# Optimization experiments

Measured on AMD Instinct MI355X. Metric: run time of the kernel, lower is better.

## Reference

```python
import jax, jax.numpy as jnp
import numpy as np

B, T, H = 2, 4096, 2048
NH, DK, DV = 16, 128, 128
CONV = 4
MLP_H = 32
EPS_STAT = 1e-6   # surprise_stat_eps
NORM_EPS = 1e-5   # o_norm eps
L2_EPS = 1e-6     # qk l2norm eps in kernel


def setup_inputs() -> dict:
    key = jax.random.key(0)
    ks = jax.random.split(key, 20)
    def w(k, shape, scale=None):
        scale = (1.0 / np.sqrt(shape[-1])) if scale is None else scale
        return jax.random.normal(k, shape, jnp.float32) * scale
    return dict(
        hidden_states=jax.random.normal(ks[0], (B, T, H), jnp.float32),
        Wq=w(ks[1], (NH * DK, H)),
        Wk=w(ks[2], (NH * DK, H)),
        Wv=w(ks[3], (NH * DV, H)),
        conv_q=w(ks[4], (NH * DK, CONV), 0.5),
        conv_k=w(ks[5], (NH * DK, CONV), 0.5),
        conv_v=w(ks[6], (NH * DV, CONV), 0.5),
        A_log=jnp.log(jax.random.uniform(ks[7], (NH,), jnp.float32, 1.0, 16.0)),
        dt_bias=jnp.zeros((NH * DK,), jnp.float32),
        Wsv=w(ks[8], (DV, DK)),
        Wb1=w(ks[9], (MLP_H, 3)), bb1=jnp.zeros((MLP_H,), jnp.float32),
        Wb2=w(ks[10], (1, MLP_H)), bb2=jnp.zeros((1,), jnp.float32),
        Wa1=w(ks[11], (MLP_H, 3)), ba1=jnp.zeros((MLP_H,), jnp.float32),
        Wa2=w(ks[12], (1, MLP_H)), ba2=jnp.zeros((1,), jnp.float32),
        Wg1=w(ks[13], (DV, H)),
        Wg2=w(ks[14], (NH * DV, DV)), bg2=jnp.zeros((NH * DV,), jnp.float32),
        norm_w=jnp.ones((DV,), jnp.float32),
        Wo=w(ks[15], (H, NH * DV)),
    )


def short_conv(x, w):
    """Causal depthwise conv1d (kernel CONV, no bias) + silu. x: [B,T,C], w: [C,CONV]."""
    K = w.shape[-1]
    xp = jnp.pad(x, ((0, 0), (K - 1, 0), (0, 0)))
    y = sum(xp[:, i:i + x.shape[1], :] * w[:, i] for i in range(K))
    return jax.nn.silu(y)


def _mlp(s, W1, b1, W2, b2):
    return (jax.nn.silu(s @ W1.T + b1) @ W2.T + b2)[..., 0]


def reference(hidden_states, Wq, Wk, Wv, conv_q, conv_k, conv_v, A_log, dt_bias,
              Wsv, Wb1, bb1, Wb2, bb2, Wa1, ba1, Wa2, ba2,
              Wg1, Wg2, bg2, norm_w, Wo):
    x = hidden_states
    Bsz, Tlen, _ = x.shape
    # projections + short conv + silu
    q = short_conv(x @ Wq.T, conv_q).reshape(Bsz, Tlen, NH, DK)
    k = short_conv(x @ Wk.T, conv_k).reshape(Bsz, Tlen, NH, DK)
    v = short_conv(x @ Wv.T, conv_v).reshape(Bsz, Tlen, NH, DV)

    # surprise proxy error stats
    v_hat = jnp.einsum('bthk,vk->bthv', k, Wsv)
    e = v_hat - v
    s_l2 = jnp.sqrt(jnp.sum(e * e, -1) + EPS_STAT)
    s_l1 = jnp.sum(jnp.abs(e), -1)
    cos_den = jnp.sqrt(jnp.sum(v_hat * v_hat, -1) + EPS_STAT) * \
              jnp.sqrt(jnp.sum(v * v, -1) + EPS_STAT) + EPS_STAT
    s_cos = 1.0 - jnp.sum(v_hat * v, -1) / cos_den
    s = jnp.stack([s_l2, s_l1, s_cos], -1)                 # [B,T,NH,3]

    beta = jax.nn.sigmoid(_mlp(s, Wb1, bb1, Wb2, bb2))      # [B,T,NH]
    amp = _mlp(s, Wa1, ba1, Wa2, ba2)                       # logit_normalizer = 1
    r = k / jnp.maximum(jnp.linalg.norm(k, axis=-1, keepdims=True), 1e-12)
    g_raw = r * amp[..., None]                              # [B,T,NH,DK]

    # KDA gate: g = -exp(A_log) * softplus(g_raw + dt_bias)
    g = -jnp.exp(A_log)[None, None, :, None] * \
        jax.nn.softplus(g_raw + dt_bias.reshape(NH, DK))

    # q/k l2-normalization inside kernel
    qn = q * jax.lax.rsqrt(jnp.sum(q * q, -1, keepdims=True) + L2_EPS)
    kn = k * jax.lax.rsqrt(jnp.sum(k * k, -1, keepdims=True) + L2_EPS)
    scale = DK ** -0.5

    def step(S, inp):
        q_t, k_t, v_t, g_t, b_t = inp                       # [B,NH,*]
        S = S * jnp.exp(g_t)[..., None]                     # per-key-dim decay, S:[B,NH,DK,DV]
        kv = jnp.einsum('bhk,bhkv->bhv', k_t, S)            # k^T S
        delta = (v_t - kv) * b_t[..., None]                 # surprise-gated delta update
        S = S + k_t[..., None] * delta[..., None, :]
        o_t = jnp.einsum('bhk,bhkv->bhv', q_t * scale, S)
        return S, o_t

    tfirst = lambda a: jnp.swapaxes(a, 0, 1)
    S0 = jnp.zeros((Bsz, NH, DK, DV), jnp.float32)
    _, o = jax.lax.scan(step, S0, (tfirst(qn), tfirst(kn), tfirst(v), tfirst(g), tfirst(beta)))
    o = jnp.swapaxes(o, 0, 1)                               # [B,T,NH,DV]

    # gated RMSNorm (sigmoid gate) + output proj
    gate = ((x @ Wg1.T) @ Wg2.T + bg2).reshape(Bsz, Tlen, NH, DV)
    o = o * jax.lax.rsqrt(jnp.mean(o * o, -1, keepdims=True) + NORM_EPS) * norm_w
    o = o * jax.nn.sigmoid(gate)
    return o.reshape(Bsz, Tlen, NH * DV) @ Wo.T
```

## Files before the change

### kernel.cpp

```cpp
#include <hip/hip_runtime.h>
#include <hip/hip_bf16.h>


typedef __attribute__((ext_vector_type(8))) short bf16x8;
typedef __attribute__((ext_vector_type(4))) short bf16x4;
typedef __attribute__((ext_vector_type(4))) float floatx4;

#define TB 4096
#define RSH 664
#define NREC 4096
#define BHSH ((size_t)NREC * RSH)
#define CSB ((size_t)16 * RSH * 2)

__device__ __forceinline__ float b2f(ushort u) {
    union { unsigned int u; float f; } c; c.u = ((unsigned int)u) << 16; return c.f;
}
__device__ __forceinline__ ushort f2b(float f) {
    union { float f; unsigned int u; } c; c.f = f;
    unsigned int r = (c.u + 0x7fffu + ((c.u >> 16) & 1u)) >> 16;
    return (ushort)r;
}
__device__ __forceinline__ float silu(float x) { return x / (1.0f + expf(-x)); }
__device__ __forceinline__ void dec8(uint4 u, float* f) {
    f[0] = __uint_as_float(u.x << 16); f[1] = __uint_as_float(u.x & 0xffff0000u);
    f[2] = __uint_as_float(u.y << 16); f[3] = __uint_as_float(u.y & 0xffff0000u);
    f[4] = __uint_as_float(u.z << 16); f[5] = __uint_as_float(u.z & 0xffff0000u);
    f[6] = __uint_as_float(u.w << 16); f[7] = __uint_as_float(u.w & 0xffff0000u);
}
__device__ __forceinline__ void dec4(uint2 u, float* f) {
    f[0] = __uint_as_float(u.x << 16); f[1] = __uint_as_float(u.x & 0xffff0000u);
    f[2] = __uint_as_float(u.y << 16); f[3] = __uint_as_float(u.y & 0xffff0000u);
}
__device__ __forceinline__ bf16x4 asbf(uint2 u) {
    union { uint2 a; bf16x4 b; } c; c.a = u; return c.b;
}

#if __has_builtin(__builtin_amdgcn_mfma_f32_16x16x16bf16_1k)
__device__ __forceinline__ floatx4 MFMA16(bf16x4 a, bf16x4 b, floatx4 c) {
    return __builtin_amdgcn_mfma_f32_16x16x16bf16_1k(a, b, c, 0, 0, 0);
}
#else
__device__ __forceinline__ floatx4 MFMA16(bf16x4 a, bf16x4 b, floatx4 c) {
    asm volatile("v_mfma_f32_16x16x16_bf16 %0, %1, %2, %0\n\ts_nop 7\n\ts_nop 7"
                 : "+v"(c) : "v"(a), "v"(b));
    return c;
}
#endif

__global__ __launch_bounds__(256) void cast_f32_bf16(const float* __restrict__ in,
                                                     ushort* __restrict__ out, int n) {
    int i = (blockIdx.x * 256 + threadIdx.x) * 4;
    int stride = gridDim.x * 256 * 4;
    for (; i + 3 < n; i += stride) {
        float4 v = *(const float4*)(in + i);
        ushort4 u;
        u.x = f2b(v.x); u.y = f2b(v.y); u.z = f2b(v.z); u.w = f2b(v.w);
        *(ushort4*)(out + i) = u;
    }
}

template <typename CT>
__global__ __launch_bounds__(256) void gemm_bf16(const ushort* __restrict__ A,
                                                 const ushort* __restrict__ B,
                                                 CT* __restrict__ C, int M, int N, int K) {
    __shared__ ushort As[128 * 40];
    __shared__ ushort Bs[128 * 40];
    const int tid = threadIdx.x;
    const int lane = tid & 63, wid = tid >> 6;
    const int wr = wid >> 1, wc = wid & 1;
    const int bm = blockIdx.y, bn = blockIdx.x;

    const int r0 = tid >> 2;
    const int kc0 = (tid & 3) * 8;
    const size_t aoff0 = (size_t)(bm * 128 + r0) * K + kc0;
    const size_t aoff1 = aoff0 + (size_t)64 * K;
    const size_t boff0 = (size_t)(bn * 128 + r0) * K + kc0;
    const size_t boff1 = boff0 + (size_t)64 * K;
    const int lw0 = r0 * 40 + kc0;
    const int lw1 = (r0 + 64) * 40 + kc0;

    const int arow = wr * 64 + (lane & 15);
    const int brow = wc * 64 + (lane & 15);
    const int kg = (lane >> 4) * 8;

    floatx4 acc[4][4];
#pragma unroll
    for (int m = 0; m < 4; ++m)
#pragma unroll
        for (int n = 0; n < 4; ++n) acc[m][n] = (floatx4){0.f, 0.f, 0.f, 0.f};

    uint4 ra0 = *(const uint4*)(A + aoff0);
    uint4 ra1 = *(const uint4*)(A + aoff1);
    uint4 rb0 = *(const uint4*)(B + boff0);
    uint4 rb1 = *(const uint4*)(B + boff1);

    for (int kt = 32; kt <= K; kt += 32) {
        __syncthreads();
        *(uint4*)(As + lw0) = ra0;
        *(uint4*)(As + lw1) = ra1;
        *(uint4*)(Bs + lw0) = rb0;
        *(uint4*)(Bs + lw1) = rb1;
        __syncthreads();
        if (kt < K) {
            ra0 = *(const uint4*)(A + aoff0 + kt);
            ra1 = *(const uint4*)(A + aoff1 + kt);
            rb0 = *(const uint4*)(B + boff0 + kt);
            rb1 = *(const uint4*)(B + boff1 + kt);
        }
        bf16x8 af[4], bfr[4];
#pragma unroll
        for (int m = 0; m < 4; ++m) af[m] = *(const bf16x8*)(As + (arow + m * 16) * 40 + kg);
#pragma unroll
        for (int n = 0; n < 4; ++n) bfr[n] = *(const bf16x8*)(Bs + (brow + n * 16) * 40 + kg);
#pragma unroll
        for (int m = 0; m < 4; ++m)
#pragma unroll
            for (int n = 0; n < 4; ++n)
                acc[m][n] = __builtin_amdgcn_mfma_f32_16x16x32_bf16(af[m], bfr[n], acc[m][n], 0, 0, 0);
    }

    const int crow0 = bm * 128 + wr * 64 + (lane >> 4) * 4;
    const int ccol0 = bn * 128 + wc * 64 + (lane & 15);
#pragma unroll
    for (int m = 0; m < 4; ++m)
#pragma unroll
        for (int n = 0; n < 4; ++n)
#pragma unroll
            for (int j = 0; j < 4; ++j) {
                int row = crow0 + m * 16 + j;
                int col = ccol0 + n * 16;
                if constexpr (sizeof(CT) == 2)
                    C[(size_t)row * N + col] = (CT)f2b(acc[m][n][j]);
                else
                    C[(size_t)row * N + col] = (CT)acc[m][n][j];
            }
}

__global__ __launch_bounds__(256) void conv_stats_kernel(
    const ushort* __restrict__ qkv,
    const float* __restrict__ convq, const float* __restrict__ convk,
    const float* __restrict__ convv, const float* __restrict__ Wsv,
    const float* __restrict__ Wb1, const float* __restrict__ bb1,
    const float* __restrict__ Wb2, const float* __restrict__ bb2,
    const float* __restrict__ Wa1, const float* __restrict__ ba1,
    const float* __restrict__ Wa2, const float* __restrict__ ba2,
    const float* __restrict__ A_log, const float* __restrict__ dt_bias,
    ushort* __restrict__ P) {
    __shared__ ushort wsv_s[128 * 136];
    __shared__ float k_sh[4][128];
    for (int i = threadIdx.x; i < 128 * 128; i += 256) {
        int row = i >> 7, col = i & 127;
        wsv_s[row * 136 + col] = f2b(Wsv[i]);
    }
    __syncthreads();
    const int wid = threadIdx.x >> 6, lane = threadIdx.x & 63;

    for (int it = 0; it < 2; ++it) {
        const int pair = blockIdx.x * 8 + it * 4 + wid;
        const int t = pair >> 4, h = pair & 15;
        const int c0 = h * 128 + 2 * lane, c1 = c0 + 1;

        float wq[4], wq2[4], wk[4], wk2[4], wv[4], wv2[4];
#pragma unroll
        for (int i2 = 0; i2 < 4; ++i2) {
            wq[i2] = convq[c0 * 4 + i2]; wq2[i2] = convq[c1 * 4 + i2];
            wk[i2] = convk[c0 * 4 + i2]; wk2[i2] = convk[c1 * 4 + i2];
            wv[i2] = convv[c0 * 4 + i2]; wv2[i2] = convv[c1 * 4 + i2];
        }
        float aq0 = 0, aq1 = 0, ak0 = 0, ak1 = 0, av0 = 0, av1 = 0;
#pragma unroll
        for (int i2 = 0; i2 < 4; ++i2) {
            int tt = t - 3 + i2;
            if (tt >= 0) {
                const ushort* rowp = qkv + (size_t)tt * 6144 + h * 128;
                uint xq = *(const uint*)(rowp + 2 * lane);
                uint xk = *(const uint*)(rowp + 2048 + 2 * lane);
                uint xv = *(const uint*)(rowp + 4096 + 2 * lane);
                aq0 = fmaf(__uint_as_float(xq << 16), wq[i2], aq0);
                aq1 = fmaf(__uint_as_float(xq & 0xffff0000u), wq2[i2], aq1);
                ak0 = fmaf(__uint_as_float(xk << 16), wk[i2], ak0);
                ak1 = fmaf(__uint_as_float(xk & 0xffff0000u), wk2[i2], ak1);
                av0 = fmaf(__uint_as_float(xv << 16), wv[i2], av0);
                av1 = fmaf(__uint_as_float(xv & 0xffff0000u), wv2[i2], av1);
            }
        }
        float q0 = silu(aq0), q1 = silu(aq1);
        float k0 = silu(ak0), k1 = silu(ak1);
        float v0 = silu(av0), v1 = silu(av1);

        __syncthreads();
        k_sh[wid][2 * lane] = k0;
        k_sh[wid][2 * lane + 1] = k1;
        __syncthreads();

        float vh0 = 0.f, vh1 = 0.f;
        const ushort* wr0 = wsv_s + (2 * lane) * 136;
        const ushort* wr1 = wsv_s + (2 * lane + 1) * 136;
#pragma unroll 4
        for (int j = 0; j < 128; j += 8) {
            float4 ka = *(const float4*)&k_sh[wid][j];
            float4 kb = *(const float4*)&k_sh[wid][j + 4];
            uint4 wa = *(const uint4*)(wr0 + j);
            uint4 wb = *(const uint4*)(wr1 + j);
            vh0 = fmaf(__uint_as_float(wa.x << 16), ka.x, vh0);
            vh0 = fmaf(__uint_as_float(wa.x & 0xffff0000u), ka.y, vh0);
            vh0 = fmaf(__uint_as_float(wa.y << 16), ka.z, vh0);
            vh0 = fmaf(__uint_as_float(wa.y & 0xffff0000u), ka.w, vh0);
            vh0 = fmaf(__uint_as_float(wa.z << 16), kb.x, vh0);
            vh0 = fmaf(__uint_as_float(wa.z & 0xffff0000u), kb.y, vh0);
            vh0 = fmaf(__uint_as_float(wa.w << 16), kb.z, vh0);
            vh0 = fmaf(__uint_as_float(wa.w & 0xffff0000u), kb.w, vh0);
            vh1 = fmaf(__uint_as_float(wb.x << 16), ka.x, vh1);
            vh1 = fmaf(__uint_as_float(wb.x & 0xffff0000u), ka.y, vh1);
            vh1 = fmaf(__uint_as_float(wb.y << 16), ka.z, vh1);
            vh1 = fmaf(__uint_as_float(wb.y & 0xffff0000u), ka.w, vh1);
            vh1 = fmaf(__uint_as_float(wb.z << 16), kb.x, vh1);
            vh1 = fmaf(__uint_as_float(wb.z & 0xffff0000u), kb.y, vh1);
            vh1 = fmaf(__uint_as_float(wb.w << 16), kb.z, vh1);
            vh1 = fmaf(__uint_as_float(wb.w & 0xffff0000u), kb.w, vh1);
        }

        float e0 = vh0 - v0, e1 = vh1 - v1;
        float se2 = e0 * e0 + e1 * e1;
        float sl1 = fabsf(e0) + fabsf(e1);
        float shv = vh0 * v0 + vh1 * v1;
        float shh = vh0 * vh0 + vh1 * vh1;
        float svv = v0 * v0 + v1 * v1;
        float sk2 = k0 * k0 + k1 * k1;
        float sq2 = q0 * q0 + q1 * q1;
#pragma unroll
        for (int m = 32; m >= 1; m >>= 1) {
            se2 += __shfl_xor(se2, m);
            sl1 += __shfl_xor(sl1, m);
            shv += __shfl_xor(shv, m);
            shh += __shfl_xor(shh, m);
            svv += __shfl_xor(svv, m);
            sk2 += __shfl_xor(sk2, m);
            sq2 += __shfl_xor(sq2, m);
        }
        float s_l2 = sqrtf(se2 + 1e-6f);
        float s_l1 = sl1;
        float s_cos = 1.0f - shv / (sqrtf(shh + 1e-6f) * sqrtf(svv + 1e-6f) + 1e-6f);

        const int j2 = lane & 31;
        const float* W1 = (lane < 32) ? Wb1 : Wa1;
        const float* b1 = (lane < 32) ? bb1 : ba1;
        const float* W2 = (lane < 32) ? Wb2 : Wa2;
        float pre = W1[j2 * 3] * s_l2 + W1[j2 * 3 + 1] * s_l1 + W1[j2 * 3 + 2] * s_cos + b1[j2];
        float val = W2[j2] * silu(pre);
#pragma unroll
        for (int m = 16; m >= 1; m >>= 1) val += __shfl_xor(val, m);
        float pre_b = __shfl(val, 0) + bb2[0];
        float pre_a = __shfl(val, 32) + ba2[0];
        float betav = 1.0f / (1.0f + expf(-pre_b));
        float amp = pre_a;

        float knorm = sqrtf(sk2);
        float rinv = amp / fmaxf(knorm, 1e-12f);
        float ah = expf(A_log[h]);
        float gr0 = fmaf(k0, rinv, dt_bias[c0]);
        float gr1 = fmaf(k1, rinv, dt_bias[c1]);
        float sp0 = (gr0 > 20.f) ? gr0 : log1pf(expf(gr0));
        float sp1 = (gr1 > 20.f) ? gr1 : log1pf(expf(gr1));

        ushort* rec = P + (size_t)h * BHSH + (size_t)t * RSH;
        float kinv = rsqrtf(sk2 + 1e-6f);
        float qinv = rsqrtf(sq2 + 1e-6f) * 0.08838834764831845f;
        *(uint*)(rec + 128 + 2 * lane) = (uint)f2b(q0 * qinv) | ((uint)f2b(q1 * qinv) << 16);
        *(uint*)(rec + 256 + 2 * lane) = (uint)f2b(k0 * kinv) | ((uint)f2b(k1 * kinv) << 16);
        *(uint*)(rec + 384 + 2 * lane) = (uint)f2b(expf(-ah * sp0)) | ((uint)f2b(expf(-ah * sp1)) << 16);
        *(uint*)(rec + 512 + 2 * lane) = (uint)f2b(v0) | ((uint)f2b(v1) << 16);
        if (lane == 0) *(float*)(rec + 640) = betav;
    }
}

__global__ __launch_bounds__(256, 1) void phasea_kernel(ushort* __restrict__ P) {
    __shared__ float lA[4][16][16];
    __shared__ float lU[4][16][16];
    __shared__ float lM[4][16][16];
    const int wid = threadIdx.x >> 6, lane = threadIdx.x & 63;
    const int g = blockIdx.x * 4 + wid;
    const int s = g >> 8, n = g & 255;
    ushort* cb = P + (size_t)s * BHSH + (size_t)n * (16 * RSH);
    char* sb = (char*)cb;
    float (*A_)[16] = lA[wid];
    float (*U_)[16] = lU[wid];
    float (*M_)[16] = lM[wid];

    float kf[32], Ef[32], qf[32], bf[16];
    uint vq[16];
#pragma unroll
    for (int i = 0; i < 16; ++i) {
        const ushort* r = cb + i * RSH;
        uint ku = *(const uint*)(r + 256 + 2 * lane);
        uint eu = *(const uint*)(r + 384 + 2 * lane);
        uint qu = *(const uint*)(r + 128 + 2 * lane);
        vq[i] = *(const uint*)(r + 512 + 2 * lane);
        bf[i] = *(const float*)(r + 640);
        kf[2 * i]     = __uint_as_float(ku << 16);
        kf[2 * i + 1] = __uint_as_float(ku & 0xffff0000u);
        Ef[2 * i]     = __uint_as_float(eu << 16);
        Ef[2 * i + 1] = __uint_as_float(eu & 0xffff0000u);
        qf[2 * i]     = __uint_as_float(qu << 16);
        qf[2 * i + 1] = __uint_as_float(qu & 0xffff0000u);
    }

    float R[32];
    float Pc0 = 1.f, Pc1 = 1.f;
#pragma unroll
    for (int i = 0; i < 16; ++i) {
#pragma unroll
        for (int j = 0; j < 16; ++j) if (j < i) {
            R[2 * j] *= Ef[2 * i];
            R[2 * j + 1] *= Ef[2 * i + 1];
        }
        float Tr[16], Ur[16];
#pragma unroll
        for (int j = 0; j < 16; ++j) { Tr[j] = 0.f; Ur[j] = 0.f; }
#pragma unroll
        for (int j = 0; j < 16; ++j) if (j < i) {
            Tr[j] = kf[2 * i] * R[2 * j] + kf[2 * i + 1] * R[2 * j + 1];
            Ur[j] = qf[2 * i] * R[2 * j] + qf[2 * i + 1] * R[2 * j + 1];
        }
        Ur[i] = qf[2 * i] * kf[2 * i] + qf[2 * i + 1] * kf[2 * i + 1];
#pragma unroll
        for (int m = 1; m <= 32; m <<= 1) {
#pragma unroll
            for (int j = 0; j < 16; ++j) if (j <= i) {
                if (j < i) Tr[j] += __shfl_xor(Tr[j], m);
                Ur[j] += __shfl_xor(Ur[j], m);
            }
        }
        if (lane == 0) {
#pragma unroll
            for (int j = 0; j < 16; ++j) if (j < i) A_[i][j] = bf[i] * Tr[j];
#pragma unroll
            for (int j = 0; j < 16; ++j) if (j <= i) U_[i][j] = Ur[j];
        }
        R[2 * i] = kf[2 * i];
        R[2 * i + 1] = kf[2 * i + 1];
        Pc0 *= Ef[2 * i];
        Pc1 *= Ef[2 * i + 1];
        *(uint*)(sb + (size_t)i * 256 + 4 * lane) =
            (uint)f2b(kf[2 * i] * Pc0) | ((uint)f2b(kf[2 * i + 1] * Pc1) << 16);
        *(uint*)(sb + 4096 + (size_t)i * 256 + 4 * lane) =
            (uint)f2b(qf[2 * i] * Pc0) | ((uint)f2b(qf[2 * i + 1] * Pc1) << 16);
    }
    *(uint*)(sb + 16384 + 4 * lane) = (uint)f2b(Pc0) | ((uint)f2b(Pc1) << 16);
    {
        uint lw[8], hw[8];
#pragma unroll
        for (int w = 0; w < 8; ++w) {
            lw[w] = (vq[2 * w] & 0xffffu) | (vq[2 * w + 1] << 16);
            hw[w] = (vq[2 * w] >> 16) | (vq[2 * w + 1] & 0xffff0000u);
        }
        char* vt0 = sb + 12288 + (size_t)(2 * lane) * 32;
        *(uint4*)(vt0)      = (uint4){lw[0], lw[1], lw[2], lw[3]};
        *(uint4*)(vt0 + 16) = (uint4){lw[4], lw[5], lw[6], lw[7]};
        *(uint4*)(vt0 + 32) = (uint4){hw[0], hw[1], hw[2], hw[3]};
        *(uint4*)(vt0 + 48) = (uint4){hw[4], hw[5], hw[6], hw[7]};
    }
    const int mcol = lane & 15;
    float M[16];
#pragma unroll
    for (int i = 0; i < 16; ++i) {
        float acc = (i == mcol) ? bf[i] : 0.f;
#pragma unroll
        for (int j = 0; j < 16; ++j) if (j < i) acc -= A_[i][j] * M[j];
        M[i] = acc;
    }
    if (lane < 16) {
#pragma unroll
        for (int j = 0; j < 16; ++j) M_[j][lane] = M[j];
    }
    if (lane < 16) {
#pragma unroll
        for (int i = 0; i < 16; ++i) {
            float acc = 0.f;
#pragma unroll
            for (int j = 0; j < 16; ++j) if (j <= i) acc += U_[i][j] * M[j];
            *(ushort*)(sb + 16640 + (size_t)i * 32 + lane * 2) = f2b(acc);
        }
    }
    {
        float kvA[16], kvB[16];
#pragma unroll
        for (int m = 0; m < 16; ++m) {
            float a0 = 0.f, a1 = 0.f;
#pragma unroll
            for (int j = 0; j < 16; ++j) if (j >= m) {
                float mv = M_[j][m];
                a0 = fmaf(mv, R[2 * j], a0);
                a1 = fmaf(mv, R[2 * j + 1], a1);
            }
            kvA[m] = a0; kvB[m] = a1;
        }
        uint wa[8], wb[8];
#pragma unroll
        for (int w = 0; w < 8; ++w) {
            wa[w] = (uint)f2b(kvA[2 * w]) | ((uint)f2b(kvA[2 * w + 1]) << 16);
            wb[w] = (uint)f2b(kvB[2 * w]) | ((uint)f2b(kvB[2 * w + 1]) << 16);
        }
        char* kt = sb + 8192 + (size_t)(2 * lane) * 32;
        *(uint4*)(kt)      = (uint4){wa[0], wa[1], wa[2], wa[3]};
        *(uint4*)(kt + 16) = (uint4){wa[4], wa[5], wa[6], wa[7]};
        *(uint4*)(kt + 32) = (uint4){wb[0], wb[1], wb[2], wb[3]};
        *(uint4*)(kt + 48) = (uint4){wb[4], wb[5], wb[6], wb[7]};
    }
}

struct FragPB { uint2 kw[8], qw[8], kvt[8], w15[8], vv, um; };

__global__ __launch_bounds__(64, 1) void phaseb_kernel(const ushort* __restrict__ P,
                                                       ushort* __restrict__ ob,
                                                       int smask, int sshift) {
    const int l = threadIdx.x;
    const int r16 = l & 15, g4 = l >> 4;
    const int s = blockIdx.x & smask, c = blockIdx.x >> sshift;
    const int b = s >> 4, h = s & 15;
    const int colbase = c * 16;
    const char* gb = (const char*)(P + (size_t)s * BHSH);
    ushort* opb = ob + (size_t)b * (TB * 2048) + h * 128 + colbase + r16;

    const int okw = r16 * 256 + g4 * 8;
    const int okvt = 8192 + r16 * 32 + g4 * 8;
    const int ow15 = 16384 + g4 * 8;
    const int ovv = 12288 + (colbase + r16) * 32 + g4 * 8;
    const int oum = 16640 + r16 * 32 + g4 * 8;

    auto ld = [&](FragPB& F, const char* sb) {
#pragma unroll
        for (int t = 0; t < 8; ++t) {
            F.kw[t]  = *(const uint2*)(sb + okw + t * 32);
            F.qw[t]  = *(const uint2*)(sb + 4096 + okw + t * 32);
            F.kvt[t] = *(const uint2*)(sb + okvt + t * 512);
            F.w15[t] = *(const uint2*)(sb + ow15 + t * 32);
        }
        F.vv = *(const uint2*)(sb + ovv);
        F.um = *(const uint2*)(sb + oum);
    };

    FragPB Fa, Fb;
    ld(Fa, gb);

    floatx4 S[8];
#pragma unroll
    for (int t = 0; t < 8; ++t) S[t] = (floatx4){0.f, 0.f, 0.f, 0.f};

    auto body = [&](int n, FragPB& F, FragPB& FN) {
        int np = n + 1; if (np > 255) np = 255;
        ld(FN, gb + (size_t)np * CSB);
        asm volatile("" ::: "memory");
        bf16x4 bs[8];
#pragma unroll
        for (int t = 0; t < 8; ++t) {
            bf16x4 v;
            v[0] = (short)f2b(S[t].x); v[1] = (short)f2b(S[t].y);
            v[2] = (short)f2b(S[t].z); v[3] = (short)f2b(S[t].w);
            bs[t] = v;
        }
        floatx4 Y = (floatx4){0.f, 0.f, 0.f, 0.f};
        floatx4 Z = (floatx4){0.f, 0.f, 0.f, 0.f};
#pragma unroll
        for (int t = 0; t < 8; ++t) {
            Y = MFMA16(asbf(F.kw[t]), bs[t], Y);
            Z = MFMA16(asbf(F.qw[t]), bs[t], Z);
        }
        float vf[4];
        dec4(F.vv, vf);
        bf16x4 rb;
        rb[0] = (short)f2b(vf[0] - Y.x); rb[1] = (short)f2b(vf[1] - Y.y);
        rb[2] = (short)f2b(vf[2] - Y.z); rb[3] = (short)f2b(vf[3] - Y.w);
        floatx4 O = MFMA16(asbf(F.um), rb, Z);
#pragma unroll
        for (int j = 0; j < 4; ++j)
            opb[(size_t)(n * 16 + g4 * 4 + j) * 2048] = f2b(O[j]);
#pragma unroll
        for (int t = 0; t < 8; ++t) {
            float wf[4];
            dec4(F.w15[t], wf);
            floatx4 Cc = (floatx4){wf[0] * S[t].x, wf[1] * S[t].y,
                                   wf[2] * S[t].z, wf[3] * S[t].w};
            S[t] = MFMA16(asbf(F.kvt[t]), rb, Cc);
        }
    };

    for (int n = 0; n < 256; n += 2) {
        body(n, Fa, Fb);
        body(n + 1, Fb, Fa);
    }
}

__global__ __launch_bounds__(256) void normgate_kernel(
    const ushort* __restrict__ o, const ushort* __restrict__ gate,
    const float* __restrict__ bg2, const float* __restrict__ norm_w,
    ushort* __restrict__ og) {
    const int lane = threadIdx.x & 63;
    const int wstart = (blockIdx.x * 256 + threadIdx.x) >> 6;
    const int nw = (gridDim.x * 256) >> 6;
    for (int pair = wstart; pair < TB * 16; pair += nw) {
        const int t = pair >> 4, h = pair & 15;
        const size_t basep = (size_t)t * 2048 + h * 128 + lane * 2;
        unsigned int ovu = *(const unsigned int*)(o + basep);
        float o0 = __uint_as_float(ovu << 16);
        float o1 = __uint_as_float(ovu & 0xffff0000u);
        float ss = o0 * o0 + o1 * o1;
#pragma unroll
        for (int m = 32; m >= 1; m >>= 1) ss += __shfl_xor(ss, m);
        float rn = rsqrtf(ss * (1.0f / 128.0f) + 1e-5f);
        const int dg = h * 128 + lane * 2;
        unsigned int gv = *(const unsigned int*)(gate + basep);
        float g0 = __uint_as_float(gv << 16) + bg2[dg];
        float g1 = __uint_as_float(gv & 0xffff0000u) + bg2[dg + 1];
        float w0 = norm_w[lane * 2], w1 = norm_w[lane * 2 + 1];
        float r0 = o0 * rn * w0 / (1.0f + expf(-g0));
        float r1 = o1 * rn * w1 / (1.0f + expf(-g1));
        unsigned int outw = (unsigned int)f2b(r0) | ((unsigned int)f2b(r1) << 16);
        *(unsigned int*)(og + basep) = outw;
    }
}

extern "C" void kernel_launch(void* const* d_in, const int* in_sizes, int n_in,
                              void* d_out, int out_size, void* d_ws, size_t ws_size,
                              hipStream_t stream) {
    const float* x = (const float*)d_in[0];
    const float* Wq = (const float*)d_in[1];
    const float* Wk = (const float*)d_in[2];
    const float* Wv = (const float*)d_in[3];
    const float* convq = (const float*)d_in[4];
    const float* convk = (const float*)d_in[5];
    const float* convv = (const float*)d_in[6];
    const float* A_log = (const float*)d_in[7];
    const float* dt_bias = (const float*)d_in[8];
    const float* Wsv = (const float*)d_in[9];
    const float* Wb1 = (const float*)d_in[10];
    const float* bb1 = (const float*)d_in[11];
    const float* Wb2 = (const float*)d_in[12];
    const float* bb2 = (const float*)d_in[13];
    const float* Wa1 = (const float*)d_in[14];
    const float* ba1 = (const float*)d_in[15];
    const float* Wa2 = (const float*)d_in[16];
    const float* ba2 = (const float*)d_in[17];
    const float* Wg1 = (const float*)d_in[18];
    const float* Wg2 = (const float*)d_in[19];
    const float* bg2 = (const float*)d_in[20];
    const float* norm_w = (const float*)d_in[21];
    const float* Wo = (const float*)d_in[22];

    const size_t PBATCH   = (size_t)16 * BHSH * 2;
    const size_t OFF_WQKV = 0;
    const size_t OFF_XB   = OFF_WQKV + 25165824;
    const size_t OFF_WG1  = OFF_XB + 16777216;
    const size_t OFF_WG2  = OFF_WG1 + 524288;
    const size_t OFF_QKV  = OFF_WG2 + 524288;
    const size_t OFF_P    = OFF_QKV + 50331648;
    const size_t NEED_B   = OFF_P + PBATCH;
    const size_t NEED_A   = OFF_P + 2 * PBATCH;
    if (ws_size < NEED_B) return;
    const bool planA = (ws_size >= NEED_A);

    char* ws = (char*)d_ws;
    ushort* wqkv = (ushort*)(ws + OFF_WQKV);
    ushort* xb   = (ushort*)(ws + OFF_XB);
    ushort* wg1b = (ushort*)(ws + OFF_WG1);
    ushort* wg2b = (ushort*)(ws + OFF_WG2);
    ushort* qkvb = (ushort*)(ws + OFF_QKV);
    ushort* P    = (ushort*)(ws + OFF_P);
    ushort* gateb = qkvb;
    ushort* xg1b  = (ushort*)(ws + OFF_QKV + 16777216);
    ushort* ogb   = (ushort*)(ws + OFF_QKV + 17825792);
    ushort* wob   = (ushort*)(ws + OFF_QKV + 34603008);
    ushort* obp = planA ? (ushort*)(ws + OFF_WQKV) : xb;

    cast_f32_bf16<<<512, 256, 0, stream>>>(Wq, wqkv, 4194304);
    cast_f32_bf16<<<512, 256, 0, stream>>>(Wk, wqkv + 4194304, 4194304);
    cast_f32_bf16<<<512, 256, 0, stream>>>(Wv, wqkv + 8388608, 4194304);
    cast_f32_bf16<<<64, 256, 0, stream>>>(Wg1, wg1b, 262144);
    cast_f32_bf16<<<64, 256, 0, stream>>>(Wg2, wg2b, 262144);

    if (planA) {
        for (int b = 0; b < 2; ++b) {
            cast_f32_bf16<<<512, 256, 0, stream>>>(x + (size_t)b * TB * 2048, xb, TB * 2048);
            gemm_bf16<ushort><<<dim3(48, TB / 128), 256, 0, stream>>>(xb, wqkv, qkvb, TB, 6144, 2048);
            conv_stats_kernel<<<TB * 16 / 8, 256, 0, stream>>>(qkvb, convq, convk, convv, Wsv,
                Wb1, bb1, Wb2, bb2, Wa1, ba1, Wa2, ba2, A_log, dt_bias,
                P + (size_t)b * 16 * BHSH);
        }
        phasea_kernel<<<2048, 256, 0, stream>>>(P);
        phaseb_kernel<<<256, 64, 0, stream>>>(P, obp, 31, 5);
        cast_f32_bf16<<<512, 256, 0, stream>>>(Wo, wob, 4194304);
        for (int b = 0; b < 2; ++b) {
            ushort* xstage = ogb;
            cast_f32_bf16<<<512, 256, 0, stream>>>(x + (size_t)b * TB * 2048, xstage, TB * 2048);
            gemm_bf16<ushort><<<dim3(1, TB / 128), 256, 0, stream>>>(xstage, wg1b, xg1b, TB, 128, 2048);
            gemm_bf16<ushort><<<dim3(16, TB / 128), 256, 0, stream>>>(xg1b, wg2b, gateb, TB, 2048, 128);
            normgate_kernel<<<2048, 256, 0, stream>>>(obp + (size_t)b * TB * 2048, gateb, bg2, norm_w, ogb);
            gemm_bf16<float><<<dim3(16, TB / 128), 256, 0, stream>>>(ogb, wob,
                (float*)d_out + (size_t)b * TB * 2048, TB, 2048, 2048);
        }
    } else {
        for (int b = 0; b < 2; ++b) {
            const float* xbp = x + (size_t)b * TB * 2048;
            float* outp = (float*)d_out + (size_t)b * TB * 2048;
            cast_f32_bf16<<<512, 256, 0, stream>>>(xbp, xb, TB * 2048);
            gemm_bf16<ushort><<<dim3(48, TB / 128), 256, 0, stream>>>(xb, wqkv, qkvb, TB, 6144, 2048);
            conv_stats_kernel<<<TB * 16 / 8, 256, 0, stream>>>(qkvb, convq, convk, convv, Wsv,
                Wb1, bb1, Wb2, bb2, Wa1, ba1, Wa2, ba2, A_log, dt_bias, P);
            gemm_bf16<ushort><<<dim3(1, TB / 128), 256, 0, stream>>>(xb, wg1b, xg1b, TB, 128, 2048);
            gemm_bf16<ushort><<<dim3(16, TB / 128), 256, 0, stream>>>(xg1b, wg2b, gateb, TB, 2048, 128);
            cast_f32_bf16<<<512, 256, 0, stream>>>(Wo, wob, 4194304);
            phasea_kernel<<<1024, 256, 0, stream>>>(P);
            phaseb_kernel<<<128, 64, 0, stream>>>(P, xb, 15, 4);
            normgate_kernel<<<2048, 256, 0, stream>>>(xb, gateb, bg2, norm_w, ogb);
            gemm_bf16<float><<<dim3(16, TB / 128), 256, 0, stream>>>(ogb, wob, outp, TB, 2048, 2048);
        }
    }
}
```

Measured before the change: 1.359 ms.

## Load GEMM tiles directly into LDS and raise phase-A occupancy bound

The bf16 GEMM now uses the direct global-to-LDS load builtin instead of staging tiles through registers. The LDS tile is unpadded (stride 32 instead of 40), which may cause bank conflicts on the MFMA fragment reads. The register prefetch of the next tile is removed, so global latency is no longer overlapped with compute. Separately, phasea_kernel's launch bounds now ask for two blocks per CU, which limits its register use.

```diff
diff --git a/kernel.cpp b/kernel.cpp
--- a/kernel.cpp
+++ b/kernel.cpp
@@ -63,8 +63,8 @@
 __global__ __launch_bounds__(256) void gemm_bf16(const ushort* __restrict__ A,
                                                  const ushort* __restrict__ B,
                                                  CT* __restrict__ C, int M, int N, int K) {
-    __shared__ ushort As[128 * 40];
-    __shared__ ushort Bs[128 * 40];
+    __shared__ ushort As[128 * 32];
+    __shared__ ushort Bs[128 * 32];
     const int tid = threadIdx.x;
     const int lane = tid & 63, wid = tid >> 6;
     const int wr = wid >> 1, wc = wid & 1;
@@ -76,8 +76,7 @@
     const size_t aoff1 = aoff0 + (size_t)64 * K;
     const size_t boff0 = (size_t)(bn * 128 + r0) * K + kc0;
     const size_t boff1 = boff0 + (size_t)64 * K;
-    const int lw0 = r0 * 40 + kc0;
-    const int lw1 = (r0 + 64) * 40 + kc0;
+    const int wbase = wid * 512;
 
     const int arow = wr * 64 + (lane & 15);
     const int brow = wc * 64 + (lane & 15);
@@ -89,29 +88,33 @@
 #pragma unroll
         for (int n = 0; n < 4; ++n) acc[m][n] = (floatx4){0.f, 0.f, 0.f, 0.f};
 
-    uint4 ra0 = *(const uint4*)(A + aoff0);
-    uint4 ra1 = *(const uint4*)(A + aoff1);
-    uint4 rb0 = *(const uint4*)(B + boff0);
-    uint4 rb1 = *(const uint4*)(B + boff1);
-
-    for (int kt = 32; kt <= K; kt += 32) {
+    for (int kt = 0; kt < K; kt += 32) {
         __syncthreads();
-        *(uint4*)(As + lw0) = ra0;
-        *(uint4*)(As + lw1) = ra1;
-        *(uint4*)(Bs + lw0) = rb0;
-        *(uint4*)(Bs + lw1) = rb1;
+#if __has_builtin(__builtin_amdgcn_global_load_lds)
+        __builtin_amdgcn_global_load_lds(
+            (const __attribute__((address_space(1))) void*)(const void*)(A + aoff0 + kt),
+            (__attribute__((address_space(3))) void*)(void*)(As + wbase), 16, 0, 0);
+        __builtin_amdgcn_global_load_lds(
+            (const __attribute__((address_space(1))) void*)(const void*)(A + aoff1 + kt),
+            (__attribute__((address_space(3))) void*)(void*)(As + 2048 + wbase), 16, 0, 0);
+        __builtin_amdgcn_global_load_lds(
+            (const __attribute__((address_space(1))) void*)(const void*)(B + boff0 + kt),
+            (__attribute__((address_space(3))) void*)(void*)(Bs + wbase), 16, 0, 0);
+        __builtin_amdgcn_global_load_lds(
+            (const __attribute__((address_space(1))) void*)(const void*)(B + boff1 + kt),
+            (__attribute__((address_space(3))) void*)(void*)(Bs + 2048 + wbase), 16, 0, 0);
+#else
+        *(uint4*)(As + tid * 8)        = *(const uint4*)(A + aoff0 + kt);
+        *(uint4*)(As + 2048 + tid * 8) = *(const uint4*)(A + aoff1 + kt);
+        *(uint4*)(Bs + tid * 8)        = *(const uint4*)(B + boff0 + kt);
+        *(uint4*)(Bs + 2048 + tid * 8) = *(const uint4*)(B + boff1 + kt);
+#endif
         __syncthreads();
-        if (kt < K) {
-            ra0 = *(const uint4*)(A + aoff0 + kt);
-            ra1 = *(const uint4*)(A + aoff1 + kt);
-            rb0 = *(const uint4*)(B + boff0 + kt);
-            rb1 = *(const uint4*)(B + boff1 + kt);
-        }
         bf16x8 af[4], bfr[4];
 #pragma unroll
-        for (int m = 0; m < 4; ++m) af[m] = *(const bf16x8*)(As + (arow + m * 16) * 40 + kg);
-#pragma unroll
-        for (int n = 0; n < 4; ++n) bfr[n] = *(const bf16x8*)(Bs + (brow + n * 16) * 40 + kg);
+        for (int m = 0; m < 4; ++m) af[m] = *(const bf16x8*)(As + (arow + m * 16) * 32 + kg);
+#pragma unroll
+        for (int n = 0; n < 4; ++n) bfr[n] = *(const bf16x8*)(Bs + (brow + n * 16) * 32 + kg);
 #pragma unroll
         for (int m = 0; m < 4; ++m)
 #pragma unroll
@@ -274,7 +277,7 @@
     }
 }
 
-__global__ __launch_bounds__(256, 1) void phasea_kernel(ushort* __restrict__ P) {
+__global__ __launch_bounds__(256, 2) void phasea_kernel(ushort* __restrict__ P) {
     __shared__ float lA[4][16][16];
     __shared__ float lU[4][16][16];
     __shared__ float lM[4][16][16];
```

After: 1.441 ms. +6.0%, slower.
